# Kernel tuning notes

Hardware: AMD Instinct MI355X
Metric: run time of the kernel (lower is better)

## Reference

```python
import jax, jax.numpy as jnp
import numpy as np

B, S, D, H = 4, 2048, 768, 12
HD = D // H
SCALE = HD ** -0.5


def setup_inputs() -> dict:
    key = jax.random.key(0)
    ks = jax.random.split(key, 10)
    inp = {
        "x": jax.random.normal(ks[0], (B, S, D), jnp.float32),
        "attn_mask": jax.random.normal(ks[1], (B, S), jnp.float32),
        "Wq": jax.random.normal(ks[2], (D, D), jnp.float32) * (D ** -0.5),
        "bq": jax.random.normal(ks[3], (D,), jnp.float32) * 0.02,
        "Wk": jax.random.normal(ks[4], (D, D), jnp.float32) * (D ** -0.5),
        "bk": jax.random.normal(ks[5], (D,), jnp.float32) * 0.02,
        "Wv": jax.random.normal(ks[6], (D, D), jnp.float32) * (D ** -0.5),
        "bv": jax.random.normal(ks[7], (D,), jnp.float32) * 0.02,
        "Wo": jax.random.normal(ks[8], (D, D), jnp.float32) * (D ** -0.5),
        "bo": jax.random.normal(ks[9], (D,), jnp.float32) * 0.02,
    }
    return inp


def _split_heads(e):
    # [B, S, D] -> [B, H, S, HD]
    return e.reshape(B, S, H, HD).transpose(0, 2, 1, 3)


def reference(x, attn_mask, Wq, bq, Wk, bk, Wv, bv, Wo, bo):
    q = _split_heads((x @ Wq + bq) * SCALE)          # [B,H,S,HD]
    k = _split_heads(x @ Wk + bk)                     # [B,H,S,HD]
    v = _split_heads(x @ Wv + bv)                     # [B,H,S,HD]
    scores = jnp.einsum('bhsd,bhtd->bhst', q, k)      # [B,H,S,S]
    scores = scores + attn_mask[:, None, None, :]     # additive mask over keys
    probs = jax.nn.softmax(scores, axis=-1)
    out = jnp.einsum('bhst,bhtd->bhsd', probs, v)     # [B,H,S,HD]
    out = out.transpose(0, 2, 1, 3).reshape(B, S, D)  # merge heads
    return out @ Wo + bo
```

## Files before the change

### kernel.cpp

```cpp
#include <hip/hip_runtime.h>
#include <cmath>

#define B_ 4
#define S_ 2048
#define D_ 768
#define H_ 12
#define HD_ 64
#define SCALE_ 0.125f
#define LOG2E_ 1.4426950408889634f
#define M_ 8192
#define NE_ 6291456ull
#define BHS_ 98304ull

typedef unsigned short ushortT;
typedef unsigned int u32;
typedef __attribute__((ext_vector_type(8))) __bf16 bf16x8;
typedef __attribute__((ext_vector_type(4))) float f32x4;
typedef __attribute__((ext_vector_type(16))) float f32x16;

typedef __attribute__((address_space(1))) const void glb_cv;
typedef __attribute__((address_space(3))) void lds_v;

__device__ inline ushortT f2bf(float f) {
    return __builtin_bit_cast(ushortT, (__bf16)f);
}

__device__ inline float bf2f(ushortT u) {
    return __builtin_bit_cast(float, (u32)u << 16);
}

__device__ inline u32 pk2bf(float a, float b) {
    return (u32)__builtin_bit_cast(ushortT, (__bf16)a)
         | ((u32)__builtin_bit_cast(ushortT, (__bf16)b) << 16);
}

__device__ inline void gload_lds16(const void* g, void* l) {
    __builtin_amdgcn_global_load_lds((glb_cv*)g, (lds_v*)l, 16, 0, 0);
}

__global__ __launch_bounds__(256)
void convert_f32_bf16(const float* __restrict__ in, ushortT* __restrict__ out)
{
    const size_t i = ((size_t)blockIdx.x * 256 + threadIdx.x) * 8;
    float4 a = *(const float4*)(in + i);
    float4 b = *(const float4*)(in + i + 4);
    union { ushortT u[8]; float4 f; } o;
    o.u[0] = f2bf(a.x); o.u[1] = f2bf(a.y); o.u[2] = f2bf(a.z); o.u[3] = f2bf(a.w);
    o.u[4] = f2bf(b.x); o.u[5] = f2bf(b.y); o.u[6] = f2bf(b.z); o.u[7] = f2bf(b.w);
    *(float4*)(out + i) = o.f;
}

__global__ __launch_bounds__(256)
void scale_mask(const float* __restrict__ in, float* __restrict__ outp)
{
    const int i = blockIdx.x * 256 + threadIdx.x;
    outp[i] = in[i] * LOG2E_;
}

__global__ __launch_bounds__(256)
void transpose_w(const float* __restrict__ W0, const float* __restrict__ W1,
                 const float* __restrict__ W2, const float* __restrict__ W3,
                 ushortT* __restrict__ wt4)
{
    const float* W = (blockIdx.z == 0) ? W0 : (blockIdx.z == 1) ? W1
                   : (blockIdx.z == 2) ? W2 : W3;
    ushortT* o = wt4 + (size_t)blockIdx.z * 768 * 768;
    __shared__ float T[64][65];
    const int tid = threadIdx.x;
    const int k0 = blockIdx.x * 64, n0 = blockIdx.y * 64;

    for (int t = tid; t < 1024; t += 256) {
        const int r = t >> 4, c4 = (t & 15) << 2;
        float4 v = *(const float4*)&W[(size_t)(k0 + r) * 768 + n0 + c4];
        T[r][c4 + 0] = v.x; T[r][c4 + 1] = v.y;
        T[r][c4 + 2] = v.z; T[r][c4 + 3] = v.w;
    }
    __syncthreads();
    for (int t = tid; t < 1024; t += 256) {
        const int r = t >> 4, c4 = (t & 15) << 2;
        union { ushortT u[4]; unsigned long long v; } ov;
        ov.u[0] = f2bf(T[c4 + 0][r]); ov.u[1] = f2bf(T[c4 + 1][r]);
        ov.u[2] = f2bf(T[c4 + 2][r]); ov.u[3] = f2bf(T[c4 + 3][r]);
        *(unsigned long long*)&o[(size_t)(n0 + r) * 768 + k0 + c4] = ov.v;
    }
}

__device__ inline void gemm_core_128x64(
    const ushortT* __restrict__ A, const ushortT* __restrict__ Bt,
    ushortT* As, ushortT* Bs, int m0, int n0, f32x4 acc[4][2])
{
    const int tid  = threadIdx.x;
    const int lane = tid & 63;
    const int wave = tid >> 6;
    const int lr = lane & 15, lg = lane >> 4;
    const int wr = wave >> 1, wc = wave & 1;

    #pragma unroll
    for (int mi = 0; mi < 4; ++mi)
        #pragma unroll
        for (int ni = 0; ni < 2; ++ni)
            acc[mi][ni] = (f32x4){0.f, 0.f, 0.f, 0.f};

    #pragma unroll 1
    for (int k0 = 0; k0 < 768; k0 += 64) {
        __syncthreads();
        #pragma unroll
        for (int it = 0; it < 4; ++it) {
            const int ci = it * 256 + tid;
            const int row = ci >> 3, c = ci & 7;
            const int sc = c ^ (row & 7);
            gload_lds16(A + (size_t)(m0 + row) * 768 + k0 + sc * 8,
                        As + (size_t)(it * 256 + wave * 64) * 8);
        }
        #pragma unroll
        for (int it = 0; it < 2; ++it) {
            const int ci = it * 256 + tid;
            const int row = ci >> 3, c = ci & 7;
            const int sc = c ^ (row & 7);
            gload_lds16(Bt + (size_t)(n0 + row) * 768 + k0 + sc * 8,
                        Bs + (size_t)(it * 256 + wave * 64) * 8);
        }
        __syncthreads();

        #pragma unroll
        for (int ks = 0; ks < 2; ++ks) {
            bf16x8 af[4], bfr[2];
            #pragma unroll
            for (int mi = 0; mi < 4; ++mi) {
                const int row = wr * 64 + mi * 16 + lr;
                const int ch = (ks * 4 + lg) ^ (row & 7);
                af[mi] = __builtin_bit_cast(bf16x8, *(const float4*)(As + row * 64 + ch * 8));
            }
            #pragma unroll
            for (int ni = 0; ni < 2; ++ni) {
                const int row = wc * 32 + ni * 16 + lr;
                const int ch = (ks * 4 + lg) ^ (row & 7);
                bfr[ni] = __builtin_bit_cast(bf16x8, *(const float4*)(Bs + row * 64 + ch * 8));
            }
            #pragma unroll
            for (int mi = 0; mi < 4; ++mi)
                #pragma unroll
                for (int ni = 0; ni < 2; ++ni)
                    acc[mi][ni] = __builtin_amdgcn_mfma_f32_16x16x32_bf16(
                        af[mi], bfr[ni], acc[mi][ni], 0, 0, 0);
        }
    }
}

__global__ __launch_bounds__(256)
void qkv_gemm(const ushortT* __restrict__ xb, const ushortT* __restrict__ wt4,
              const float* __restrict__ bq, const float* __restrict__ bk,
              const float* __restrict__ bv,
              ushortT* __restrict__ qb, ushortT* __restrict__ kb,
              ushortT* __restrict__ vtb)
{
    __shared__ __align__(16) ushortT As[128 * 64];
    __shared__ __align__(16) ushortT Bs[64 * 64];
    const int z = blockIdx.z;
    const ushortT* Wt = wt4 + (size_t)z * 768 * 768;
    const float* bias = (z == 0) ? bq : (z == 1) ? bk : bv;
    const float scale = (z == 0) ? (SCALE_ * LOG2E_) : 1.0f;

    const int m0 = blockIdx.x * 128, n0 = blockIdx.y * 64;
    f32x4 acc[4][2];
    gemm_core_128x64(xb, Wt, As, Bs, m0, n0, acc);

    const int tid = threadIdx.x;
    const int lane = tid & 63, wave = tid >> 6;
    const int lr = lane & 15, lg = lane >> 4;
    const int wr = wave >> 1, wc = wave & 1;
    const int h = n0 >> 6;

    if (z == 2) {
        #pragma unroll
        for (int ni = 0; ni < 2; ++ni) {
            const int nn = wc * 32 + ni * 16 + lr;
            const float bb = bias[n0 + nn];
            #pragma unroll
            for (int mi = 0; mi < 4; ++mi) {
                const int mb = m0 + wr * 64 + mi * 16 + lg * 4;
                const int b = mb >> 11, s = mb & 2047;
                ushort4 ov;
                ov.x = f2bf(acc[mi][ni][0] + bb);
                ov.y = f2bf(acc[mi][ni][1] + bb);
                ov.z = f2bf(acc[mi][ni][2] + bb);
                ov.w = f2bf(acc[mi][ni][3] + bb);
                *(ushort4*)&vtb[(((size_t)b * H_ + h) * HD_ + nn) * S_ + s] = ov;
            }
        }
    } else {
        ushortT* out = (z == 0) ? qb : kb;
        #pragma unroll
        for (int ni = 0; ni < 2; ++ni) {
            const int nn = wc * 32 + ni * 16 + lr;
            const float bb = bias[n0 + nn];
            #pragma unroll
            for (int mi = 0; mi < 4; ++mi) {
                #pragma unroll
                for (int j = 0; j < 4; ++j) {
                    const int m = m0 + wr * 64 + mi * 16 + lg * 4 + j;
                    const int b = m >> 11, s = m & 2047;
                    out[(((size_t)b * H_ + h) * S_ + s) * HD_ + nn] =
                        f2bf((acc[mi][ni][j] + bb) * scale);
                }
            }
        }
    }
}

__global__ __launch_bounds__(256)
void o_gemm(const ushortT* __restrict__ ab, const ushortT* __restrict__ wto,
            const float* __restrict__ bo, float* __restrict__ out)
{
    __shared__ __align__(16) ushortT As[128 * 64];
    __shared__ __align__(16) ushortT Bs[64 * 64];
    const int m0 = blockIdx.x * 128, n0 = blockIdx.y * 64;
    f32x4 acc[4][2];
    gemm_core_128x64(ab, wto, As, Bs, m0, n0, acc);

    const int tid = threadIdx.x;
    const int lane = tid & 63, wave = tid >> 6;
    const int lr = lane & 15, lg = lane >> 4;
    const int wr = wave >> 1, wc = wave & 1;

    #pragma unroll
    for (int ni = 0; ni < 2; ++ni) {
        const int n = n0 + wc * 32 + ni * 16 + lr;
        const float bb = bo[n];
        #pragma unroll
        for (int mi = 0; mi < 4; ++mi) {
            #pragma unroll
            for (int j = 0; j < 4; ++j) {
                const int m = m0 + wr * 64 + mi * 16 + lg * 4 + j;
                out[(size_t)m * 768 + n] = acc[mi][ni][j] + bb;
            }
        }
    }
}

__global__ __launch_bounds__(256, 3)
void attn_mfma(const ushortT* __restrict__ Q, const ushortT* __restrict__ K,
               const ushortT* __restrict__ Vt, const float* __restrict__ msc,
               ushortT* __restrict__ pn, float* __restrict__ pl)
{
    __shared__ __align__(16) ushortT Ks[2][64 * 64];
    __shared__ __align__(16) ushortT Vs[2][64 * 64];

    const int tid  = threadIdx.x;
    const int lane = tid & 63;
    const int wq   = tid >> 6;
    const int col  = lane & 31;
    const int hi   = lane >> 5;

    const int gid  = blockIdx.x;
    const int xcd  = gid & 7;
    const int w    = gid >> 3;
    const int bh_i = xcd * 6 + (w >> 5);
    const int r5   = w & 31;
    const int q0   = (r5 >> 1) * 128;
    const int kh   = r5 & 1;
    const int b    = bh_i / H_;
    const int h    = bh_i % H_;
    const size_t bh = (size_t)bh_i;

    bf16x8 qf[4];
    {
        const ushortT* Qg = Q + (bh * S_ + q0 + wq * 32 + col) * HD_;
        #pragma unroll
        for (int ks = 0; ks < 4; ++ks)
            qf[ks] = __builtin_bit_cast(bf16x8,
                *(const float4*)(Qg + ks * 16 + hi * 8));
    }

    const ushortT* Kg = K  + bh * S_ * HD_ + (size_t)kh * 1024 * HD_;
    const ushortT* Vg = Vt + bh * HD_ * S_ + (size_t)kh * 1024;
    const float*   mg = msc + (size_t)b * S_ + (size_t)kh * 1024;

    const ushortT* ksrc[2];
    const ushortT* vsrc[2];
    #pragma unroll
    for (int it = 0; it < 2; ++it) {
        const int ci = it * 256 + tid;
        const int row = ci >> 3, c = ci & 7, sc = c ^ (row & 7);
        ksrc[it] = Kg + (size_t)row * HD_ + sc * 8;
        vsrc[it] = Vg + (size_t)row * S_ + sc * 8;
    }

    int ko[2][4], vo[2][4];
    #pragma unroll
    for (int kb2 = 0; kb2 < 2; ++kb2) {
        const int r = kb2 * 32 + col;
        #pragma unroll
        for (int ks = 0; ks < 4; ++ks)
            ko[kb2][ks] = r * 128 + (((2 * ks + hi) ^ (r & 7)) << 4);
    }
    #pragma unroll
    for (int hb = 0; hb < 2; ++hb) {
        const int r = hb * 32 + col;
        #pragma unroll
        for (int sg = 0; sg < 4; ++sg)
            vo[hb][sg] = r * 128 + (((2 * sg + hi) ^ (r & 7)) << 4);
    }

    bf16x8 onesA;
    #pragma unroll
    for (int i = 0; i < 8; ++i) onesA[i] = (__bf16)1.0f;

    f32x16 acc[2];
    f32x16 accl;
    #pragma unroll
    for (int hb = 0; hb < 2; ++hb)
        #pragma unroll
        for (int r = 0; r < 16; ++r) acc[hb][r] = 0.f;
    #pragma unroll
    for (int r = 0; r < 16; ++r) accl[r] = 0.f;

    auto stage = [&](int bsel) {
        #pragma unroll
        for (int it = 0; it < 2; ++it) {
            gload_lds16(ksrc[it], &Ks[bsel][(it * 256 + wq * 64) * 8]);
            ksrc[it] += 64 * HD_;
        }
        #pragma unroll
        for (int it = 0; it < 2; ++it) {
            gload_lds16(vsrc[it], &Vs[bsel][(it * 256 + wq * 64) * 8]);
            vsrc[it] += 64;
        }
    };

    stage(0);
    __syncthreads();

    for (int kt = 0; kt < 16; ++kt) {
        const int buf = kt & 1;
        if (kt + 1 < 16) stage(buf ^ 1);

        u32 bw[4][4];
        #pragma unroll
        for (int kb2 = 0; kb2 < 2; ++kb2) {
            f32x16 s;
            #pragma unroll
            for (int g = 0; g < 4; ++g) {
                float4 mv = *(const float4*)(mg + kt * 64 + kb2 * 32 + g * 8 + hi * 4);
                s[4 * g + 0] = mv.x;
                s[4 * g + 1] = mv.y;
                s[4 * g + 2] = mv.z;
                s[4 * g + 3] = mv.w;
            }

            __builtin_amdgcn_s_setprio(1);
            #pragma unroll
            for (int ks = 0; ks < 4; ++ks) {
                bf16x8 kf = __builtin_bit_cast(bf16x8,
                    *(const float4*)((const char*)&Ks[buf][0] + ko[kb2][ks]));
                s = __builtin_amdgcn_mfma_f32_32x32x16_bf16(
                    kf, qf[ks], s, 0, 0, 0);
            }
            __builtin_amdgcn_s_setprio(0);

            float p[16];
            #pragma unroll
            for (int r = 0; r < 16; ++r) p[r] = exp2f(s[r]);

            #pragma unroll
            for (int sl = 0; sl < 2; ++sl) {
                u32 u0 = pk2bf(p[8 * sl + 0], p[8 * sl + 1]);
                u32 u1 = pk2bf(p[8 * sl + 2], p[8 * sl + 3]);
                u32 v0 = pk2bf(p[8 * sl + 4], p[8 * sl + 5]);
                u32 v1 = pk2bf(p[8 * sl + 6], p[8 * sl + 7]);
                asm("v_permlane32_swap_b32 %0, %1" : "+v"(u0), "+v"(v0));
                asm("v_permlane32_swap_b32 %0, %1" : "+v"(u1), "+v"(v1));
                const int sg = kb2 * 2 + sl;
                bw[sg][0] = u0; bw[sg][1] = u1;
                bw[sg][2] = v0; bw[sg][3] = v1;
            }
        }

        __builtin_amdgcn_s_setprio(1);
        #pragma unroll
        for (int sg = 0; sg < 4; ++sg) {
            union { u32 w[4]; bf16x8 v; } pb;
            pb.w[0] = bw[sg][0]; pb.w[1] = bw[sg][1];
            pb.w[2] = bw[sg][2]; pb.w[3] = bw[sg][3];
            #pragma unroll
            for (int hb = 0; hb < 2; ++hb) {
                bf16x8 vf = __builtin_bit_cast(bf16x8,
                    *(const float4*)((const char*)&Vs[buf][0] + vo[hb][sg]));
                acc[hb] = __builtin_amdgcn_mfma_f32_32x32x16_bf16(
                    vf, pb.v, acc[hb], 0, 0, 0);
            }
            accl = __builtin_amdgcn_mfma_f32_32x32x16_bf16(
                onesA, pb.v, accl, 0, 0, 0);
        }
        __builtin_amdgcn_s_setprio(0);

        __syncthreads();
    }

    ushortT* pnh = pn + (size_t)kh * NE_;
    float*   plh = pl + (size_t)kh * BHS_;
    const int q = q0 + wq * 32 + col;
    const size_t row = (size_t)b * S_ + q;
    plh[bh * S_ + q] = accl[0];
    #pragma unroll
    for (int hb = 0; hb < 2; ++hb) {
        #pragma unroll
        for (int t = 0; t < 4; ++t) {
            ushort4 ov;
            ov.x = f2bf(acc[hb][4 * t + 0]);
            ov.y = f2bf(acc[hb][4 * t + 1]);
            ov.z = f2bf(acc[hb][4 * t + 2]);
            ov.w = f2bf(acc[hb][4 * t + 3]);
            *(ushort4*)&pnh[row * D_ + h * HD_ + hb * 32 + t * 8 + hi * 4] = ov;
        }
    }
}

__global__ __launch_bounds__(256)
void combine(const ushortT* __restrict__ pn, const float* __restrict__ pl,
             ushortT* __restrict__ ab)
{
    const size_t i8 = ((size_t)blockIdx.x * 256 + threadIdx.x) * 8;
    const int d   = (int)(i8 % D_);
    const size_t row = i8 / D_;
    const int hh  = d >> 6;
    const int b   = (int)(row >> 11);
    const int s   = (int)(row & 2047);
    const size_t li = ((size_t)b * H_ + hh) * S_ + s;
    const float inv = 1.f / (pl[li] + pl[BHS_ + li]);

    union { ushortT u[8]; float4 f; } a, c, o;
    a.f = *(const float4*)(pn + i8);
    c.f = *(const float4*)(pn + NE_ + i8);
    #pragma unroll
    for (int j = 0; j < 8; ++j)
        o.u[j] = f2bf((bf2f(a.u[j]) + bf2f(c.u[j])) * inv);
    *(float4*)(ab + i8) = o.f;
}

extern "C" void kernel_launch(void* const* d_in, const int* in_sizes, int n_in,
                              void* d_out, int out_size, void* d_ws, size_t ws_size,
                              hipStream_t stream)
{
    const float* x    = (const float*)d_in[0];
    const float* mask = (const float*)d_in[1];
    const float* Wq   = (const float*)d_in[2];
    const float* bq   = (const float*)d_in[3];
    const float* Wk   = (const float*)d_in[4];
    const float* bk   = (const float*)d_in[5];
    const float* Wv   = (const float*)d_in[6];
    const float* bv   = (const float*)d_in[7];
    const float* Wo   = (const float*)d_in[8];
    const float* bo   = (const float*)d_in[9];
    float* out = (float*)d_out;

    ushortT* xb  = (ushortT*)d_ws;
    ushortT* qb  = xb + NE_;
    ushortT* kb  = qb + NE_;
    ushortT* vtb = kb + NE_;
    ushortT* pn  = vtb + NE_;
    ushortT* wt4 = pn + 2 * NE_;
    float*   msc = (float*)(wt4 + (size_t)4 * 768 * 768);
    float*   pl  = msc + (size_t)B_ * S_;
    ushortT* ab  = xb;

    convert_f32_bf16<<<NE_ / 2048, 256, 0, stream>>>(x, xb);
    scale_mask<<<(B_ * S_) / 256, 256, 0, stream>>>(mask, msc);
    transpose_w<<<dim3(12, 12, 4), 256, 0, stream>>>(Wq, Wk, Wv, Wo, wt4);

    qkv_gemm<<<dim3(M_ / 128, 12, 3), 256, 0, stream>>>(
        xb, wt4, bq, bk, bv, qb, kb, vtb);

    attn_mfma<<<1536, 256, 0, stream>>>(qb, kb, vtb, msc, pn, pl);

    combine<<<NE_ / 2048, 256, 0, stream>>>(pn, pl, ab);

    o_gemm<<<dim3(M_ / 128, 12), 256, 0, stream>>>(
        ab, wt4 + (size_t)3 * 768 * 768, bo, out);
}
```

Measured before the change: 175.8 us.

## Halve attention key tile to 32 and raise occupancy to six blocks

The attention kernel now streams K/V in 32-key tiles instead of 64, halving LDS per block and the per-iteration register footprint (one score tile, two P fragments). The launch bound goes from 3 to 6 blocks per CU so more waves can hide latency. In exchange the loop runs twice as many iterations, each with its own __syncthreads, and the staging and swizzle indexing are rewritten for the narrower V tile.

New measurement: 289.2 us. 1.65x slower.

```diff
diff --git a/kernel.cpp b/kernel.cpp
--- a/kernel.cpp
+++ b/kernel.cpp
@@ -238,13 +238,13 @@
     }
 }
 
-__global__ __launch_bounds__(256, 3)
+__global__ __launch_bounds__(256, 6)
 void attn_mfma(const ushortT* __restrict__ Q, const ushortT* __restrict__ K,
                const ushortT* __restrict__ Vt, const float* __restrict__ msc,
                ushortT* __restrict__ pn, float* __restrict__ pl)
 {
-    __shared__ __align__(16) ushortT Ks[2][64 * 64];
-    __shared__ __align__(16) ushortT Vs[2][64 * 64];
+    __shared__ __align__(16) ushortT Ks[2][32 * 64];
+    __shared__ __align__(16) ushortT Vs[2][64 * 32];
 
     const int tid  = threadIdx.x;
     const int lane = tid & 63;
@@ -276,30 +276,28 @@
     const ushortT* Vg = Vt + bh * HD_ * S_ + (size_t)kh * 1024;
     const float*   mg = msc + (size_t)b * S_ + (size_t)kh * 1024;
 
-    const ushortT* ksrc[2];
-    const ushortT* vsrc[2];
-    #pragma unroll
-    for (int it = 0; it < 2; ++it) {
-        const int ci = it * 256 + tid;
-        const int row = ci >> 3, c = ci & 7, sc = c ^ (row & 7);
-        ksrc[it] = Kg + (size_t)row * HD_ + sc * 8;
-        vsrc[it] = Vg + (size_t)row * S_ + sc * 8;
-    }
-
-    int ko[2][4], vo[2][4];
-    #pragma unroll
-    for (int kb2 = 0; kb2 < 2; ++kb2) {
-        const int r = kb2 * 32 + col;
+    const ushortT* ksrc;
+    const ushortT* vsrc;
+    {
+        const int kr = tid >> 3, kc = tid & 7, ksc = kc ^ (kr & 7);
+        ksrc = Kg + (size_t)kr * HD_ + ksc * 8;
+        const int vr = tid >> 2, vc = tid & 3, vsc = vc ^ (vr & 3);
+        vsrc = Vg + (size_t)vr * S_ + vsc * 8;
+    }
+
+    int ko[4], vo[2][2];
+    {
+        const int r = col;
         #pragma unroll
         for (int ks = 0; ks < 4; ++ks)
-            ko[kb2][ks] = r * 128 + (((2 * ks + hi) ^ (r & 7)) << 4);
+            ko[ks] = r * 128 + (((2 * ks + hi) ^ (r & 7)) << 4);
     }
     #pragma unroll
     for (int hb = 0; hb < 2; ++hb) {
         const int r = hb * 32 + col;
         #pragma unroll
-        for (int sg = 0; sg < 4; ++sg)
-            vo[hb][sg] = r * 128 + (((2 * sg + hi) ^ (r & 7)) << 4);
+        for (int sg = 0; sg < 2; ++sg)
+            vo[hb][sg] = r * 64 + (((2 * sg + hi) ^ (r & 3)) << 4);
     }
 
     bf16x8 onesA;
@@ -316,69 +314,59 @@
     for (int r = 0; r < 16; ++r) accl[r] = 0.f;
 
     auto stage = [&](int bsel) {
-        #pragma unroll
-        for (int it = 0; it < 2; ++it) {
-            gload_lds16(ksrc[it], &Ks[bsel][(it * 256 + wq * 64) * 8]);
-            ksrc[it] += 64 * HD_;
-        }
-        #pragma unroll
-        for (int it = 0; it < 2; ++it) {
-            gload_lds16(vsrc[it], &Vs[bsel][(it * 256 + wq * 64) * 8]);
-            vsrc[it] += 64;
-        }
+        gload_lds16(ksrc, &Ks[bsel][(size_t)wq * 512]);
+        ksrc += 32 * HD_;
+        gload_lds16(vsrc, &Vs[bsel][(size_t)wq * 512]);
+        vsrc += 32;
     };
 
     stage(0);
     __syncthreads();
 
-    for (int kt = 0; kt < 16; ++kt) {
+    for (int kt = 0; kt < 32; ++kt) {
         const int buf = kt & 1;
-        if (kt + 1 < 16) stage(buf ^ 1);
-
-        u32 bw[4][4];
-        #pragma unroll
-        for (int kb2 = 0; kb2 < 2; ++kb2) {
-            f32x16 s;
-            #pragma unroll
-            for (int g = 0; g < 4; ++g) {
-                float4 mv = *(const float4*)(mg + kt * 64 + kb2 * 32 + g * 8 + hi * 4);
-                s[4 * g + 0] = mv.x;
-                s[4 * g + 1] = mv.y;
-                s[4 * g + 2] = mv.z;
-                s[4 * g + 3] = mv.w;
-            }
-
-            __builtin_amdgcn_s_setprio(1);
-            #pragma unroll
-            for (int ks = 0; ks < 4; ++ks) {
-                bf16x8 kf = __builtin_bit_cast(bf16x8,
-                    *(const float4*)((const char*)&Ks[buf][0] + ko[kb2][ks]));
-                s = __builtin_amdgcn_mfma_f32_32x32x16_bf16(
-                    kf, qf[ks], s, 0, 0, 0);
-            }
-            __builtin_amdgcn_s_setprio(0);
-
-            float p[16];
-            #pragma unroll
-            for (int r = 0; r < 16; ++r) p[r] = exp2f(s[r]);
-
-            #pragma unroll
-            for (int sl = 0; sl < 2; ++sl) {
-                u32 u0 = pk2bf(p[8 * sl + 0], p[8 * sl + 1]);
-                u32 u1 = pk2bf(p[8 * sl + 2], p[8 * sl + 3]);
-                u32 v0 = pk2bf(p[8 * sl + 4], p[8 * sl + 5]);
-                u32 v1 = pk2bf(p[8 * sl + 6], p[8 * sl + 7]);
-                asm("v_permlane32_swap_b32 %0, %1" : "+v"(u0), "+v"(v0));
-                asm("v_permlane32_swap_b32 %0, %1" : "+v"(u1), "+v"(v1));
-                const int sg = kb2 * 2 + sl;
-                bw[sg][0] = u0; bw[sg][1] = u1;
-                bw[sg][2] = v0; bw[sg][3] = v1;
-            }
+        if (kt + 1 < 32) stage(buf ^ 1);
+
+        f32x16 s;
+        #pragma unroll
+        for (int g = 0; g < 4; ++g) {
+            float4 mv = *(const float4*)(mg + kt * 32 + g * 8 + hi * 4);
+            s[4 * g + 0] = mv.x;
+            s[4 * g + 1] = mv.y;
+            s[4 * g + 2] = mv.z;
+            s[4 * g + 3] = mv.w;
         }
 
         __builtin_amdgcn_s_setprio(1);
         #pragma unroll
-        for (int sg = 0; sg < 4; ++sg) {
+        for (int ks = 0; ks < 4; ++ks) {
+            bf16x8 kf = __builtin_bit_cast(bf16x8,
+                *(const float4*)((const char*)&Ks[buf][0] + ko[ks]));
+            s = __builtin_amdgcn_mfma_f32_32x32x16_bf16(
+                kf, qf[ks], s, 0, 0, 0);
+        }
+        __builtin_amdgcn_s_setprio(0);
+
+        float p[16];
+        #pragma unroll
+        for (int r = 0; r < 16; ++r) p[r] = exp2f(s[r]);
+
+        u32 bw[2][4];
+        #pragma unroll
+        for (int sl = 0; sl < 2; ++sl) {
+            u32 u0 = pk2bf(p[8 * sl + 0], p[8 * sl + 1]);
+            u32 u1 = pk2bf(p[8 * sl + 2], p[8 * sl + 3]);
+            u32 v0 = pk2bf(p[8 * sl + 4], p[8 * sl + 5]);
+            u32 v1 = pk2bf(p[8 * sl + 6], p[8 * sl + 7]);
+            asm("v_permlane32_swap_b32 %0, %1" : "+v"(u0), "+v"(v0));
+            asm("v_permlane32_swap_b32 %0, %1" : "+v"(u1), "+v"(v1));
+            bw[sl][0] = u0; bw[sl][1] = u1;
+            bw[sl][2] = v0; bw[sl][3] = v1;
+        }
+
+        __builtin_amdgcn_s_setprio(1);
+        #pragma unroll
+        for (int sg = 0; sg < 2; ++sg) {
             union { u32 w[4]; bf16x8 v; } pb;
             pb.w[0] = bw[sg][0]; pb.w[1] = bw[sg][1];
             pb.w[2] = bw[sg][2]; pb.w[3] = bw[sg][3];
```
